# Kernel optimization log

Measured on AMD Instinct MI355X. Metric: run time of the kernel, lower is better.

The kernel has to match this reference:

```python
import jax, jax.numpy as jnp
import numpy as np

B, N, S, K, R = 4, 8192, 2048, 64, 0.2  # batch, points, centroids, neighbors, ball radius
EPS = 1e-5  # BatchNorm eps


def fps_indices(x, n_samples):
    """Farthest point sampling; returns int32 [B, n_samples] indices."""
    xs = jax.lax.stop_gradient(x)
    Bb, Nn, _ = xs.shape

    def step(carry, _):
        dist, farthest = carry
        centroid = jnp.take_along_axis(xs, farthest[:, None, None], axis=1)  # [B,1,3]
        d = jnp.sum((xs - centroid) ** 2, axis=-1)  # [B,N]
        dist = jnp.minimum(dist, d)
        nxt = jnp.argmax(dist, axis=-1).astype(jnp.int32)
        return (dist, nxt), farthest

    init = (jnp.full((Bb, Nn), 1e10, xs.dtype), jnp.zeros((Bb,), jnp.int32))
    _, idxs = jax.lax.scan(step, init, None, length=n_samples)  # [S,B]
    return jnp.transpose(idxs)  # [B,S]


def ball_query(x, centroids, radius, k):
    """First k point indices within radius of each centroid, -1 padded. int32 [B,S,k]."""
    xs = jax.lax.stop_gradient(x)
    cs = jax.lax.stop_gradient(centroids)
    Nn = xs.shape[1]
    d2 = jnp.sum((cs[:, :, None, :] - xs[:, None, :, :]) ** 2, axis=-1)  # [B,S,N]
    cand = jnp.where(d2 < radius * radius, jnp.arange(Nn, dtype=jnp.int32), Nn)
    neg_topk, _ = jax.lax.top_k(-cand, k)  # k smallest candidate indices
    idx = -neg_topk
    return jnp.where(idx == Nn, -1, idx)


def _forward(x, x_complete, layers, idx_fps, idx_ball):
    centroids = jnp.take_along_axis(x, idx_fps[..., None], axis=1)  # [B,S,3]
    valid = idx_ball >= 0  # [B,S,K]
    sidx = jnp.maximum(idx_ball, 0)
    gather = lambda pts: jax.vmap(lambda p, i: p[i])(pts, sidx)  # [B,S,K,C]
    x_local = gather(x) - centroids[:, :, None, :]  # relative coords
    feats = jnp.concatenate([gather(x_complete), x_local], axis=-1)  # [B,S,K,67]
    h = feats.reshape(B, S * K, -1).transpose(0, 2, 1)  # [B,67,S*K]
    for (W, b, g, bt, m, v) in layers:  # Conv1d(k=1) -> BN(eval) -> ReLU
        h = jnp.einsum('oc,bcn->bon', W, h) + b[None, :, None]
        h = (h - m[None, :, None]) * (g * jax.lax.rsqrt(v + EPS))[None, :, None] + bt[None, :, None]
        h = jax.nn.relu(h)
    h = h.reshape(B, -1, S, K)  # [B,128,S,K]
    h = jnp.where(valid[:, None, :, :], h, -jnp.inf)  # mask invalid neighbors
    pooled = jnp.max(h, axis=3)  # masked max pool over neighborhood
    return centroids, pooled.transpose(0, 2, 1)  # [B,S,3], [B,S,128]


def setup_inputs():
    key = jax.random.key(0)
    ks = jax.random.split(key, 8)
    x = jax.random.uniform(ks[0], (B, N, 3), jnp.float32)
    x_complete = jax.random.normal(ks[1], (B, N, 64), jnp.float32)
    dims = [67, 64, 64, 128]
    inp = {'x': x, 'x_complete': x_complete}
    for i in range(3):
        cin, cout = dims[i], dims[i + 1]
        kk = jax.random.split(ks[2 + i], 6)
        inp[f'W{i+1}'] = jax.random.normal(kk[0], (cout, cin), jnp.float32) * 0.05
        inp[f'b{i+1}'] = jax.random.normal(kk[1], (cout,), jnp.float32) * 0.02
        inp[f'g{i+1}'] = 1.0 + 0.1 * jax.random.normal(kk[2], (cout,), jnp.float32)
        inp[f'bt{i+1}'] = jax.random.normal(kk[3], (cout,), jnp.float32) * 0.02
        inp[f'm{i+1}'] = jax.random.normal(kk[4], (cout,), jnp.float32) * 0.05
        inp[f'v{i+1}'] = jax.random.uniform(kk[5], (cout,), jnp.float32, minval=0.5, maxval=1.5)
    return inp


def reference(x, x_complete, W1, b1, g1, bt1, m1, v1, W2, b2, g2, bt2, m2, v2, W3, b3, g3, bt3, m3, v3):
    idx_fps = fps_indices(x, S)
    cen_sg = jnp.take_along_axis(jax.lax.stop_gradient(x), idx_fps[..., None], axis=1)
    idx_ball = ball_query(x, cen_sg, R, K)
    layers = ((W1, b1, g1, bt1, m1, v1), (W2, b2, g2, bt2, m2, v2), (W3, b3, g3, bt3, m3, v3))
    return _forward(x, x_complete, layers, idx_fps, idx_ball)
```

## Files before the change

### kernel.cpp

```cpp
#include <hip/hip_runtime.h>
#include <math.h>

#define BATCH 4
#define NPTS  8192
#define NSAMP 2048
#define KNBR  64
#define EPSF  1e-5f

typedef float v2f __attribute__((ext_vector_type(2)));

__global__ void prep_kernel(const float* __restrict__ W1, const float* __restrict__ W2,
                            const float* __restrict__ W3,
                            float* __restrict__ W1t, float* __restrict__ W2t,
                            float* __restrict__ W3t) {
    int t = threadIdx.x;
    for (int i = t; i < 64 * 67; i += 256) { int o = i / 67, c = i % 67; W1t[c * 64 + o] = W1[i]; }
    for (int i = t; i < 64 * 64; i += 256) { int o = i >> 6, c = i & 63; W2t[c * 64 + o] = W2[i]; }
    for (int i = t; i < 128 * 64; i += 256) { int o = i >> 6, c = i & 63; W3t[c * 128 + o] = W3[i]; }
}

#define DPP_FMAX(v, ctrl)                                                            \
    do {                                                                             \
        int _t = __builtin_amdgcn_update_dpp(0, __float_as_int(v), ctrl, 0xf, 0xf, true); \
        (v) = fmaxf((v), __int_as_float(_t));                                        \
    } while (0)

__global__ __launch_bounds__(512) void fps_kernel(const float* __restrict__ x,
                                                  float* __restrict__ cen_out) {
#pragma clang fp contract(off)
    const int b = blockIdx.x;
    const int tid = threadIdx.x;
    const int lane = tid & 63;
    const int wid = tid >> 6;
    __shared__ float sx[NPTS], sy[NPTS], sz[NPTS];
    __shared__ __align__(16) float pd[2][8];
    __shared__ int pi[2];
    __shared__ int hist[NSAMP];

    const float* xb = x + (size_t)b * NPTS * 3;
    for (int i = tid; i < NPTS; i += 512) {
        sx[i] = xb[3 * i + 0];
        sy[i] = xb[3 * i + 1];
        sz[i] = xb[3 * i + 2];
    }
    if (tid == 0) { pi[0] = 0x7fffffff; pi[1] = 0x7fffffff; }
    __syncthreads();

    v2f px[8], py[8], pz[8], dist[8];
#pragma unroll
    for (int j = 0; j < 8; j++) {
        int p = tid * 16 + 2 * j;
        px[j] = (v2f){sx[p], sx[p + 1]};
        py[j] = (v2f){sy[p], sy[p + 1]};
        pz[j] = (v2f){sz[p], sz[p + 1]};
        dist[j] = (v2f){1e10f, 1e10f};
    }

    int cur = 0;
    for (int s = 0; s < NSAMP; s++) {
        float cx = sx[cur], cy = sy[cur], cz = sz[cur];
        if (tid == 0) hist[s] = cur;
        const v2f cvx = (v2f){cx, cx}, cvy = (v2f){cy, cy}, cvz = (v2f){cz, cz};
        v2f m = (v2f){-1.0f, -1.0f};
#pragma unroll
        for (int j = 0; j < 8; j++) {
            v2f dx = px[j] - cvx;
            v2f dy = py[j] - cvy;
            v2f dz = pz[j] - cvz;
            v2f d = ((dx * dx) + (dy * dy)) + (dz * dz);
            v2f dm;
            dm.x = fminf(dist[j].x, d.x);
            dm.y = fminf(dist[j].y, d.y);
            dist[j] = dm;
            m.x = fmaxf(m.x, dm.x);
            m.y = fmaxf(m.y, dm.y);
        }
        float bestd = fmaxf(m.x, m.y);
        float w = bestd;
        DPP_FMAX(w, 0x111);
        DPP_FMAX(w, 0x112);
        DPP_FMAX(w, 0x114);
        DPP_FMAX(w, 0x118);
        DPP_FMAX(w, 0x142);
        DPP_FMAX(w, 0x143);
        const int p = s & 1;
        if (lane == 63) pd[p][wid] = w;
        __syncthreads();
        float4 da = *(const float4*)&pd[p][0];
        float4 db = *(const float4*)&pd[p][4];
        float bmax = fmaxf(fmaxf(fmaxf(da.x, da.y), fmaxf(da.z, da.w)),
                           fmaxf(fmaxf(db.x, db.y), fmaxf(db.z, db.w)));
        if (tid == 0) pi[1 - p] = 0x7fffffff;
        int local = 0x7fffffff;
#pragma unroll
        for (int j = 0; j < 8; j++) {
            if (dist[j].x == bmax) local = min(local, tid * 16 + 2 * j);
            if (dist[j].y == bmax) local = min(local, tid * 16 + 2 * j + 1);
        }
        if (local != 0x7fffffff) atomicMin(&pi[p], local);
        __syncthreads();
        cur = pi[p];
    }

    __syncthreads();
    for (int i = tid; i < NSAMP; i += 512) {
        int idx = hist[i];
        float* o = cen_out + ((size_t)b * NSAMP + i) * 3;
        o[0] = sx[idx]; o[1] = sy[idx]; o[2] = sz[idx];
    }
}

__global__ __launch_bounds__(256) void ball_kernel(const float* __restrict__ x,
                                                   const float* __restrict__ cen,
                                                   int* __restrict__ idxb) {
    const int wid = threadIdx.x >> 6, lane = threadIdx.x & 63;
    const int id = blockIdx.x * 4 + wid;
    const int b = id >> 11;
    const float r2 = (float)(0.2 * 0.2);
    const float cx = cen[3 * id], cy = cen[3 * id + 1], cz = cen[3 * id + 2];
    const float* xb = x + (size_t)b * NPTS * 3;

    int count = 0;
    for (int base = 0; base < NPTS && count < KNBR; base += 64) {
        int p = base + lane;
        float pxv = xb[3 * p], pyv = xb[3 * p + 1], pzv = xb[3 * p + 2];
        float dx = __fsub_rn(cx, pxv);
        float dy = __fsub_rn(cy, pyv);
        float dz = __fsub_rn(cz, pzv);
        float d2 = __fadd_rn(__fadd_rn(__fmul_rn(dx, dx), __fmul_rn(dy, dy)), __fmul_rn(dz, dz));
        bool hit = d2 < r2;
        unsigned long long m = __ballot(hit);
        if (hit) {
            int pos = count + __popcll(m & ((1ull << lane) - 1ull));
            if (pos < KNBR) idxb[(size_t)id * KNBR + pos] = p;
        }
        count += (int)__popcll(m);
    }
    for (int pos = count + lane; pos < KNBR; pos += 64)
        idxb[(size_t)id * KNBR + pos] = -1;
}

__global__ __launch_bounds__(256) void mlp_kernel(
    const float* __restrict__ x, const float* __restrict__ xc,
    const float* __restrict__ cen, const int* __restrict__ idxb,
    const float* __restrict__ W1t, const float* __restrict__ b1, const float* __restrict__ g1,
    const float* __restrict__ bt1, const float* __restrict__ m1, const float* __restrict__ v1,
    const float* __restrict__ W2t, const float* __restrict__ b2, const float* __restrict__ g2,
    const float* __restrict__ bt2, const float* __restrict__ m2, const float* __restrict__ v2,
    const float* __restrict__ W3t, const float* __restrict__ b3, const float* __restrict__ g3,
    const float* __restrict__ bt3, const float* __restrict__ m3, const float* __restrict__ v3,
    float* __restrict__ pooled) {
    const int wid = threadIdx.x >> 6, lane = threadIdx.x & 63;
    const int id = blockIdx.x * 4 + wid;
    const int b = id >> 11;
    __shared__ float sred[4][64][33];

    int il = idxb[(size_t)id * KNBR + lane];
    bool valid = il >= 0;
    int ik = valid ? il : 0;

    float cx = cen[3 * id], cy = cen[3 * id + 1], cz = cen[3 * id + 2];
    const float* xp = x + ((size_t)b * NPTS + ik) * 3;
    const float* xcp = xc + ((size_t)b * NPTS + ik) * 64;

    float h1[64];
#pragma unroll
    for (int o = 0; o < 64; o++) h1[o] = 0.f;
#pragma unroll
    for (int c4 = 0; c4 < 16; c4++) {
        float4 t = ((const float4*)xcp)[c4];
        float tv0 = t.x, tv1 = t.y, tv2 = t.z, tv3 = t.w;
#pragma unroll
        for (int o = 0; o < 64; o++) h1[o] = fmaf(W1t[(c4 * 4 + 0) * 64 + o], tv0, h1[o]);
#pragma unroll
        for (int o = 0; o < 64; o++) h1[o] = fmaf(W1t[(c4 * 4 + 1) * 64 + o], tv1, h1[o]);
#pragma unroll
        for (int o = 0; o < 64; o++) h1[o] = fmaf(W1t[(c4 * 4 + 2) * 64 + o], tv2, h1[o]);
#pragma unroll
        for (int o = 0; o < 64; o++) h1[o] = fmaf(W1t[(c4 * 4 + 3) * 64 + o], tv3, h1[o]);
    }
    {
        float xl0 = xp[0] - cx, xl1 = xp[1] - cy, xl2 = xp[2] - cz;
#pragma unroll
        for (int o = 0; o < 64; o++) h1[o] = fmaf(W1t[64 * 64 + o], xl0, h1[o]);
#pragma unroll
        for (int o = 0; o < 64; o++) h1[o] = fmaf(W1t[65 * 64 + o], xl1, h1[o]);
#pragma unroll
        for (int o = 0; o < 64; o++) h1[o] = fmaf(W1t[66 * 64 + o], xl2, h1[o]);
    }
#pragma unroll
    for (int o = 0; o < 64; o++) {
        float sc = g1[o] * rsqrtf(v1[o] + EPSF);
        h1[o] = fmaxf(fmaf(h1[o] + b1[o] - m1[o], sc, bt1[o]), 0.f);
    }

    float h2[64];
#pragma unroll
    for (int o = 0; o < 64; o++) h2[o] = 0.f;
#pragma unroll
    for (int c = 0; c < 64; c++) {
        float hv = h1[c];
#pragma unroll
        for (int o = 0; o < 64; o++) h2[o] = fmaf(W2t[c * 64 + o], hv, h2[o]);
    }
#pragma unroll
    for (int o = 0; o < 64; o++) {
        float sc = g2[o] * rsqrtf(v2[o] + EPSF);
        h2[o] = fmaxf(fmaf(h2[o] + b2[o] - m2[o], sc, bt2[o]), 0.f);
    }

    for (int ch = 0; ch < 4; ch++) {
        float acc[32];
#pragma unroll
        for (int oo = 0; oo < 32; oo++) acc[oo] = 0.f;
#pragma unroll
        for (int c = 0; c < 64; c++) {
            float hv = h2[c];
#pragma unroll
            for (int oo = 0; oo < 32; oo++)
                acc[oo] = fmaf(W3t[c * 128 + ch * 32 + oo], hv, acc[oo]);
        }
#pragma unroll
        for (int oo = 0; oo < 32; oo++) {
            int o = ch * 32 + oo;
            float sc = g3[o] * rsqrtf(v3[o] + EPSF);
            float t = fmaxf(fmaf(acc[oo] + b3[o] - m3[o], sc, bt3[o]), 0.f);
            sred[wid][lane][oo] = valid ? t : -INFINITY;
        }
        __syncthreads();
        {
            int c = lane & 31, half = lane >> 5;
            float mx = -INFINITY;
#pragma unroll
            for (int r = 0; r < 32; r++) mx = fmaxf(mx, sred[wid][half * 32 + r][c]);
            mx = fmaxf(mx, __shfl_xor(mx, 32, 64));
            if (lane < 32) pooled[(size_t)id * 128 + ch * 32 + c] = mx;
        }
        __syncthreads();
    }
}

extern "C" void kernel_launch(void* const* d_in, const int* in_sizes, int n_in,
                              void* d_out, int out_size, void* d_ws, size_t ws_size,
                              hipStream_t stream) {
    const float* x  = (const float*)d_in[0];
    const float* xc = (const float*)d_in[1];
    const float* W1 = (const float*)d_in[2];
    const float* b1 = (const float*)d_in[3];
    const float* g1 = (const float*)d_in[4];
    const float* bt1 = (const float*)d_in[5];
    const float* m1 = (const float*)d_in[6];
    const float* v1 = (const float*)d_in[7];
    const float* W2 = (const float*)d_in[8];
    const float* b2 = (const float*)d_in[9];
    const float* g2 = (const float*)d_in[10];
    const float* bt2 = (const float*)d_in[11];
    const float* m2 = (const float*)d_in[12];
    const float* v2 = (const float*)d_in[13];
    const float* W3 = (const float*)d_in[14];
    const float* b3 = (const float*)d_in[15];
    const float* g3 = (const float*)d_in[16];
    const float* bt3 = (const float*)d_in[17];
    const float* m3 = (const float*)d_in[18];
    const float* v3 = (const float*)d_in[19];

    float* out = (float*)d_out;
    float* cen = out;
    float* pooled = out + (size_t)BATCH * NSAMP * 3;

    int* idxb = (int*)d_ws;
    float* W1t = (float*)((char*)d_ws + (size_t)BATCH * NSAMP * KNBR * 4);
    float* W2t = W1t + 67 * 64;
    float* W3t = W2t + 64 * 64;

    prep_kernel<<<1, 256, 0, stream>>>(W1, W2, W3, W1t, W2t, W3t);
    fps_kernel<<<BATCH, 512, 0, stream>>>(x, cen);
    ball_kernel<<<(BATCH * NSAMP) / 4, 256, 0, stream>>>(x, cen, idxb);
    mlp_kernel<<<(BATCH * NSAMP) / 4, 256, 0, stream>>>(
        x, xc, cen, idxb,
        W1t, b1, g1, bt1, m1, v1,
        W2t, b2, g2, bt2, m2, v2,
        W3t, b3, g3, bt3, m3, v3,
        pooled);
}
```

Baseline: 2.419 ms.

## Spatially sort FPS points into Morton cells and skip distant thread blocks

```diff
diff --git a/kernel.cpp b/kernel.cpp
--- a/kernel.cpp
+++ b/kernel.cpp
@@ -8,6 +8,8 @@
 #define EPSF  1e-5f
 
 typedef float v2f __attribute__((ext_vector_type(2)));
+typedef unsigned long long u64;
+typedef unsigned short u16;
 
 __global__ void prep_kernel(const float* __restrict__ W1, const float* __restrict__ W2,
                             const float* __restrict__ W3,
@@ -25,88 +27,130 @@
         (v) = fmaxf((v), __int_as_float(_t));                                        \
     } while (0)
 
+__device__ inline int spread3(int v) { return ((v & 4) << 4) | ((v & 2) << 2) | (v & 1); }
+
 __global__ __launch_bounds__(512) void fps_kernel(const float* __restrict__ x,
                                                   float* __restrict__ cen_out) {
 #pragma clang fp contract(off)
     const int b = blockIdx.x;
     const int tid = threadIdx.x;
-    const int lane = tid & 63;
-    const int wid = tid >> 6;
-    __shared__ float sx[NPTS], sy[NPTS], sz[NPTS];
-    __shared__ __align__(16) float pd[2][8];
-    __shared__ int pi[2];
-    __shared__ int hist[NSAMP];
+
+    __shared__ float sxs[NPTS], sys[NPTS], szs[NPTS];
+    __shared__ u16 buf[NPTS];
+    __shared__ u16 hist[NSAMP];
+    __shared__ unsigned int cnt[512];
+    __shared__ u64 slot[3];
+    __shared__ int pos0s;
 
     const float* xb = x + (size_t)b * NPTS * 3;
-    for (int i = tid; i < NPTS; i += 512) {
-        sx[i] = xb[3 * i + 0];
-        sy[i] = xb[3 * i + 1];
-        sz[i] = xb[3 * i + 2];
-    }
-    if (tid == 0) { pi[0] = 0x7fffffff; pi[1] = 0x7fffffff; }
+
+    float lx[16], ly[16], lz[16];
+    int key[16];
+#pragma unroll
+    for (int j = 0; j < 16; j++) {
+        int oi = tid + 512 * j;
+        lx[j] = xb[3 * oi + 0];
+        ly[j] = xb[3 * oi + 1];
+        lz[j] = xb[3 * oi + 2];
+        int ix = min(7, max(0, (int)(lx[j] * 8.0f)));
+        int iy = min(7, max(0, (int)(ly[j] * 8.0f)));
+        int iz = min(7, max(0, (int)(lz[j] * 8.0f)));
+        key[j] = (spread3(ix) << 2) | (spread3(iy) << 1) | spread3(iz);
+    }
+    if (tid < 512) cnt[tid] = 0;
+    if (tid == 0) { slot[0] = 0; slot[1] = 0; slot[2] = 0; }
+    __syncthreads();
+#pragma unroll
+    for (int j = 0; j < 16; j++) atomicAdd(&cnt[key[j]], 1u);
+    __syncthreads();
+    if (tid == 0) {
+        unsigned int run = 0;
+        for (int k = 0; k < 512; k++) { unsigned int c = cnt[k]; cnt[k] = run; run += c; }
+    }
+    __syncthreads();
+#pragma unroll
+    for (int j = 0; j < 16; j++) {
+        int oi = tid + 512 * j;
+        unsigned int pos = atomicAdd(&cnt[key[j]], 1u);
+        sxs[pos] = lx[j]; sys[pos] = ly[j]; szs[pos] = lz[j];
+        buf[pos] = (u16)oi;
+        if (oi == 0) pos0s = (int)pos;
+    }
     __syncthreads();
 
     v2f px[8], py[8], pz[8], dist[8];
+    int oi[16];
+    float bnx = 1e30f, bny = 1e30f, bnz = 1e30f, bxx = -1e30f, bxy = -1e30f, bxz = -1e30f;
 #pragma unroll
     for (int j = 0; j < 8; j++) {
         int p = tid * 16 + 2 * j;
-        px[j] = (v2f){sx[p], sx[p + 1]};
-        py[j] = (v2f){sy[p], sy[p + 1]};
-        pz[j] = (v2f){sz[p], sz[p + 1]};
+        float x0 = sxs[p], x1 = sxs[p + 1];
+        float y0 = sys[p], y1 = sys[p + 1];
+        float z0 = szs[p], z1 = szs[p + 1];
+        px[j] = (v2f){x0, x1}; py[j] = (v2f){y0, y1}; pz[j] = (v2f){z0, z1};
         dist[j] = (v2f){1e10f, 1e10f};
-    }
-
-    int cur = 0;
+        oi[2 * j] = buf[p]; oi[2 * j + 1] = buf[p + 1];
+        bnx = fminf(bnx, fminf(x0, x1)); bxx = fmaxf(bxx, fmaxf(x0, x1));
+        bny = fminf(bny, fminf(y0, y1)); bxy = fmaxf(bxy, fmaxf(y0, y1));
+        bnz = fminf(bnz, fminf(z0, z1)); bxz = fmaxf(bxz, fmaxf(z0, z1));
+    }
+    int curpos = pos0s;
+    float tmax = 1e10f;
+    __syncthreads();
+
+    int p3 = 0;
     for (int s = 0; s < NSAMP; s++) {
-        float cx = sx[cur], cy = sy[cur], cz = sz[cur];
-        if (tid == 0) hist[s] = cur;
-        const v2f cvx = (v2f){cx, cx}, cvy = (v2f){cy, cy}, cvz = (v2f){cz, cz};
-        v2f m = (v2f){-1.0f, -1.0f};
-#pragma unroll
-        for (int j = 0; j < 8; j++) {
-            v2f dx = px[j] - cvx;
-            v2f dy = py[j] - cvy;
-            v2f dz = pz[j] - cvz;
-            v2f d = ((dx * dx) + (dy * dy)) + (dz * dz);
-            v2f dm;
-            dm.x = fminf(dist[j].x, d.x);
-            dm.y = fminf(dist[j].y, d.y);
-            dist[j] = dm;
-            m.x = fmaxf(m.x, dm.x);
-            m.y = fmaxf(m.y, dm.y);
-        }
-        float bestd = fmaxf(m.x, m.y);
-        float w = bestd;
-        DPP_FMAX(w, 0x111);
-        DPP_FMAX(w, 0x112);
-        DPP_FMAX(w, 0x114);
-        DPP_FMAX(w, 0x118);
-        DPP_FMAX(w, 0x142);
-        DPP_FMAX(w, 0x143);
-        const int p = s & 1;
-        if (lane == 63) pd[p][wid] = w;
+        if (tid == 0) hist[s] = (u16)curpos;
+        float cx = sxs[curpos], cy = sys[curpos], cz = szs[curpos];
+        float dlx = fmaxf(fmaxf(__fsub_rn(bnx, cx), __fsub_rn(cx, bxx)), 0.f);
+        float dly = fmaxf(fmaxf(__fsub_rn(bny, cy), __fsub_rn(cy, bxy)), 0.f);
+        float dlz = fmaxf(fmaxf(__fsub_rn(bnz, cz), __fsub_rn(cz, bxz)), 0.f);
+        float lb2 = dlx * dlx + dly * dly + dlz * dlz;
+        if (!(lb2 > tmax * 1.0001f)) {
+            const v2f cvx = (v2f){cx, cx}, cvy = (v2f){cy, cy}, cvz = (v2f){cz, cz};
+            v2f m = (v2f){-1.0f, -1.0f};
+#pragma unroll
+            for (int j = 0; j < 8; j++) {
+                v2f dx = px[j] - cvx;
+                v2f dy = py[j] - cvy;
+                v2f dz = pz[j] - cvz;
+                v2f d = ((dx * dx) + (dy * dy)) + (dz * dz);
+                v2f dm;
+                dm.x = fminf(dist[j].x, d.x);
+                dm.y = fminf(dist[j].y, d.y);
+                dist[j] = dm;
+                m.x = fmaxf(m.x, dm.x);
+                m.y = fmaxf(m.y, dm.y);
+            }
+            tmax = fmaxf(m.x, m.y);
+        }
+        float w = tmax;
+        DPP_FMAX(w, 0x111); DPP_FMAX(w, 0x112); DPP_FMAX(w, 0x114);
+        DPP_FMAX(w, 0x118); DPP_FMAX(w, 0x142); DPP_FMAX(w, 0x143);
+        float wmax = __int_as_float(__builtin_amdgcn_readlane(__float_as_int(w), 63));
+        if (tmax == wmax) {
+            int mi = 0x7fffffff, mp = 0;
+#pragma unroll
+            for (int j = 0; j < 8; j++) {
+                if (dist[j].x == wmax && oi[2 * j] < mi)     { mi = oi[2 * j];     mp = tid * 16 + 2 * j; }
+                if (dist[j].y == wmax && oi[2 * j + 1] < mi) { mi = oi[2 * j + 1]; mp = tid * 16 + 2 * j + 1; }
+            }
+            u64 k = ((u64)__float_as_uint(wmax) << 32) |
+                    ((u64)(unsigned)(8191 - mi) << 13) | (u64)(unsigned)mp;
+            atomicMax(&slot[p3], k);
+        }
+        int pn = p3 + 1; if (pn == 3) pn = 0;
+        if (tid == 0) slot[pn] = 0;
         __syncthreads();
-        float4 da = *(const float4*)&pd[p][0];
-        float4 db = *(const float4*)&pd[p][4];
-        float bmax = fmaxf(fmaxf(fmaxf(da.x, da.y), fmaxf(da.z, da.w)),
-                           fmaxf(fmaxf(db.x, db.y), fmaxf(db.z, db.w)));
-        if (tid == 0) pi[1 - p] = 0x7fffffff;
-        int local = 0x7fffffff;
-#pragma unroll
-        for (int j = 0; j < 8; j++) {
-            if (dist[j].x == bmax) local = min(local, tid * 16 + 2 * j);
-            if (dist[j].y == bmax) local = min(local, tid * 16 + 2 * j + 1);
-        }
-        if (local != 0x7fffffff) atomicMin(&pi[p], local);
-        __syncthreads();
-        cur = pi[p];
+        curpos = (int)(slot[p3] & 0x1fff);
+        p3 = pn;
     }
 
     __syncthreads();
     for (int i = tid; i < NSAMP; i += 512) {
-        int idx = hist[i];
+        int pos = hist[i];
         float* o = cen_out + ((size_t)b * NSAMP + i) * 3;
-        o[0] = sx[idx]; o[1] = sy[idx]; o[2] = sz[idx];
+        o[0] = sxs[pos]; o[1] = sys[pos]; o[2] = szs[pos];
     }
 }
 
```

New measurement: 3.281 ms. 35.6% more time.

## Replace atomicMin argmax with ballot-based per-wave winner and single barrier

Applied to the files above, without the earlier changes.

```diff
diff --git a/kernel.cpp b/kernel.cpp
--- a/kernel.cpp
+++ b/kernel.cpp
@@ -33,8 +33,8 @@
     const int lane = tid & 63;
     const int wid = tid >> 6;
     __shared__ float sx[NPTS], sy[NPTS], sz[NPTS];
-    __shared__ __align__(16) float pd[2][8];
-    __shared__ int pi[2];
+    __shared__ __align__(16) float pdist[2][8];
+    __shared__ __align__(16) float4 pcoord[2][8];
     __shared__ int hist[NSAMP];
 
     const float* xb = x + (size_t)b * NPTS * 3;
@@ -43,7 +43,6 @@
         sy[i] = xb[3 * i + 1];
         sz[i] = xb[3 * i + 2];
     }
-    if (tid == 0) { pi[0] = 0x7fffffff; pi[1] = 0x7fffffff; }
     __syncthreads();
 
     v2f px[8], py[8], pz[8], dist[8];
@@ -57,8 +56,8 @@
     }
 
     int cur = 0;
+    float cx = sx[0], cy = sy[0], cz = sz[0];
     for (int s = 0; s < NSAMP; s++) {
-        float cx = sx[cur], cy = sy[cur], cz = sz[cur];
         if (tid == 0) hist[s] = cur;
         const v2f cvx = (v2f){cx, cx}, cvy = (v2f){cy, cy}, cvz = (v2f){cz, cz};
         v2f m = (v2f){-1.0f, -1.0f};
@@ -68,12 +67,9 @@
             v2f dy = py[j] - cvy;
             v2f dz = pz[j] - cvz;
             v2f d = ((dx * dx) + (dy * dy)) + (dz * dz);
-            v2f dm;
-            dm.x = fminf(dist[j].x, d.x);
-            dm.y = fminf(dist[j].y, d.y);
+            v2f dm = __builtin_elementwise_min(dist[j], d);
             dist[j] = dm;
-            m.x = fmaxf(m.x, dm.x);
-            m.y = fmaxf(m.y, dm.y);
+            m = __builtin_elementwise_max(m, dm);
         }
         float bestd = fmaxf(m.x, m.y);
         float w = bestd;
@@ -83,23 +79,33 @@
         DPP_FMAX(w, 0x118);
         DPP_FMAX(w, 0x142);
         DPP_FMAX(w, 0x143);
+        float wmax = __int_as_float(__builtin_amdgcn_readlane(__float_as_int(w), 63));
+        unsigned long long eq = __ballot(bestd == wmax);
+        int src = __ffsll(eq) - 1;
         const int p = s & 1;
-        if (lane == 63) pd[p][wid] = w;
+        if (lane == src) {
+            float wx = 0.f, wy = 0.f, wz = 0.f; int wi = 0;
+#pragma unroll
+            for (int j = 7; j >= 0; j--) {
+                if (dist[j].y == wmax) { wx = px[j].y; wy = py[j].y; wz = pz[j].y; wi = tid * 16 + 2 * j + 1; }
+                if (dist[j].x == wmax) { wx = px[j].x; wy = py[j].x; wz = pz[j].x; wi = tid * 16 + 2 * j; }
+            }
+            pcoord[p][wid] = (float4){wx, wy, wz, __int_as_float(wi)};
+            pdist[p][wid] = wmax;
+        }
         __syncthreads();
-        float4 da = *(const float4*)&pd[p][0];
-        float4 db = *(const float4*)&pd[p][4];
-        float bmax = fmaxf(fmaxf(fmaxf(da.x, da.y), fmaxf(da.z, da.w)),
-                           fmaxf(fmaxf(db.x, db.y), fmaxf(db.z, db.w)));
-        if (tid == 0) pi[1 - p] = 0x7fffffff;
-        int local = 0x7fffffff;
-#pragma unroll
-        for (int j = 0; j < 8; j++) {
-            if (dist[j].x == bmax) local = min(local, tid * 16 + 2 * j);
-            if (dist[j].y == bmax) local = min(local, tid * 16 + 2 * j + 1);
-        }
-        if (local != 0x7fffffff) atomicMin(&pi[p], local);
-        __syncthreads();
-        cur = pi[p];
+        float4 d0 = *(const float4*)&pdist[p][0];
+        float4 d1 = *(const float4*)&pdist[p][4];
+        int w01 = (d0.y > d0.x) ? 1 : 0; float m01 = fmaxf(d0.x, d0.y);
+        int w23 = (d0.w > d0.z) ? 3 : 2; float m23 = fmaxf(d0.z, d0.w);
+        int w45 = (d1.y > d1.x) ? 5 : 4; float m45 = fmaxf(d1.x, d1.y);
+        int w67 = (d1.w > d1.z) ? 7 : 6; float m67 = fmaxf(d1.z, d1.w);
+        int wa = (m23 > m01) ? w23 : w01; float ma = fmaxf(m01, m23);
+        int wb = (m67 > m45) ? w67 : w45; float mb = fmaxf(m45, m67);
+        int ww = (mb > ma) ? wb : wa;
+        float4 win = pcoord[p][ww];
+        cx = win.x; cy = win.y; cz = win.z;
+        cur = __float_as_int(win.w);
     }
 
     __syncthreads();
```

Result: slower. 3.534 ms (+46.1%).
